# Kernel tuning notes

Hardware: AMD Instinct MI355X
Metric: run time of the kernel (lower is better)

## Reference

```python
import jax, jax.numpy as jnp
import numpy as np

B, S, D, H = 2, 2048, 1024, 16
DK = D // H

def setup_inputs() -> dict:
    key = jax.random.key(0)
    ks = jax.random.split(key, 12)
    def lin(k):
        kw, kb = jax.random.split(k)
        bound = 1.0 / np.sqrt(D)
        W = jax.random.uniform(kw, (D, D), jnp.float32, -bound, bound)
        b = jax.random.uniform(kb, (D,), jnp.float32, -bound, bound)
        return W, b
    Wq, bq = lin(ks[0]); Wk, bk = lin(ks[1]); Wv, bv = lin(ks[2]); Wo, bo = lin(ks[3])
    q = jax.random.normal(ks[4], (B, S, D), jnp.float32)
    k = jax.random.normal(ks[5], (B, S, D), jnp.float32)
    v = jax.random.normal(ks[6], (B, S, D), jnp.float32)
    mask = jnp.ones((1, 1, S, S), jnp.int32)
    return {"q": q, "k": k, "v": v, "mask": mask,
            "Wq": Wq, "bq": bq, "Wk": Wk, "bk": bk,
            "Wv": Wv, "bv": bv, "Wo": Wo, "bo": bo}

def reference(q, k, v, mask, Wq, bq, Wk, bk, Wv, bv, Wo, bo):
    # torch Linear: y = x @ W.T + b
    Q = (q @ Wq.T + bq).reshape(B, S, H, DK).transpose(0, 2, 1, 3)  # [B,H,S,DK]
    K = (k @ Wk.T + bk).reshape(B, S, H, DK).transpose(0, 2, 1, 3)
    V = (v @ Wv.T + bv).reshape(B, S, H, DK).transpose(0, 2, 1, 3)
    scores = jnp.einsum('bhqd,bhkd->bhqk', Q, K) / jnp.sqrt(jnp.float32(DK))
    scores = jnp.where(mask == 0, jnp.float32(-1e9), scores)
    attn = jax.nn.softmax(scores, axis=-1)
    context = jnp.einsum('bhqk,bhkd->bhqd', attn, V)  # [B,H,S,DK]
    concat = context.transpose(0, 2, 1, 3).reshape(B, S, D)
    return concat @ Wo.T + bo
```

## Files before the change

kernel.cpp:

```cpp
#include <hip/hip_runtime.h>
#include <hip/hip_bf16.h>

#define BB 2
#define SS 2048
#define DD 1024
#define HH 16
#define DKK 64

typedef __hip_bfloat16 bf16;
typedef unsigned short u16;
using frag_ab = __attribute__((ext_vector_type(8))) short;
using frag_cd = __attribute__((ext_vector_type(4))) float;

__device__ inline u16 f2bf(float f) {
    bf16 h = __float2bfloat16(f);
    return *reinterpret_cast<u16*>(&h);
}

__device__ inline void gld16(const void* g, void* l) {
    __builtin_amdgcn_global_load_lds((const __attribute__((address_space(1))) void*)g,
                                     (__attribute__((address_space(3))) void*)l,
                                     16, 0, 0);
}

__device__ inline int swz16(int idx) {
    return idx ^ (((idx >> 6) & 7) << 3);
}

__global__ __launch_bounds__(256) void prep(
    const float* __restrict__ q, const float* __restrict__ k, const float* __restrict__ v,
    const float* __restrict__ Wq, const float* __restrict__ Wk,
    const float* __restrict__ Wv, const float* __restrict__ Wo,
    u16* __restrict__ qb, u16* __restrict__ kb, u16* __restrict__ vb,
    u16* __restrict__ Wqb, u16* __restrict__ Wkb, u16* __restrict__ Wvb, u16* __restrict__ Wob,
    const int* __restrict__ mask, int* __restrict__ flags) {
    int bid = blockIdx.x;
    int t = threadIdx.x;
    if (bid < 8192) {
        const float* src;
        u16* dst;
        int local;
        if (bid < 6144) {
            int ts = bid >> 11;
            local = bid & 2047;
            src = ts == 0 ? q : (ts == 1 ? k : v);
            dst = ts == 0 ? qb : (ts == 1 ? kb : vb);
        } else {
            int wsel = (bid - 6144) >> 9;
            local = (bid - 6144) & 511;
            src = wsel == 0 ? Wq : (wsel == 1 ? Wk : (wsel == 2 ? Wv : Wo));
            dst = wsel == 0 ? Wqb : (wsel == 1 ? Wkb : (wsel == 2 ? Wvb : Wob));
        }
        size_t base = (size_t)local * 2048 + t * 8;
        float4 a = *(const float4*)&src[base];
        float4 b = *(const float4*)&src[base + 4];
        ushort4 u0, u1;
        u0.x = f2bf(a.x); u0.y = f2bf(a.y); u0.z = f2bf(a.z); u0.w = f2bf(a.w);
        u1.x = f2bf(b.x); u1.y = f2bf(b.y); u1.z = f2bf(b.z); u1.w = f2bf(b.w);
        *(ushort4*)&dst[base] = u0;
        *(ushort4*)&dst[base + 4] = u1;
    } else {
        int tile = bid - 8192;
        int qt = tile >> 5, kt = tile & 31;
        __shared__ int f;
        if (t == 0) f = 0;
        __syncthreads();
        int qq = qt * 64 + (t >> 2);
        const int4* row = (const int4*)(mask + (size_t)qq * SS + kt * 64 + (t & 3) * 16);
        int anyz = 0;
#pragma unroll
        for (int i = 0; i < 4; ++i) {
            int4 m4 = row[i];
            anyz |= (m4.x == 0) | (m4.y == 0) | (m4.z == 0) | (m4.w == 0);
        }
        if (anyz) f = 1;
        __syncthreads();
        if (t == 0) flags[tile] = f;
    }
}

__global__ __launch_bounds__(256) void qkv_gemm(
    const u16* __restrict__ Aq, const u16* __restrict__ Ak, const u16* __restrict__ Av,
    const u16* __restrict__ Wq, const u16* __restrict__ Wk, const u16* __restrict__ Wv,
    const float* __restrict__ bq, const float* __restrict__ bk, const float* __restrict__ bv,
    u16* __restrict__ Qo, u16* __restrict__ Ko, u16* __restrict__ Vo) {
    __shared__ u16 As[128 * 32];
    __shared__ u16 Bs[128 * 32];

    int z = blockIdx.z;
    const u16* A = z == 0 ? Aq : (z == 1 ? Ak : Av);
    const u16* W = z == 0 ? Wq : (z == 1 ? Wk : Wv);
    const float* bias = z == 0 ? bq : (z == 1 ? bk : bv);
    u16* out = z == 0 ? Qo : (z == 1 ? Ko : Vo);

    int t = threadIdx.x;
    int m0 = blockIdx.y * 128;
    int n0 = blockIdx.x * 128;
    int w = t >> 6, lane = t & 63;
    int quad = lane >> 4, l16 = lane & 15;
    int wm = w >> 1, wn = w & 1;

    const u16* Ab = A + (size_t)m0 * DD;
    const u16* Wb = W + (size_t)n0 * DD;

    frag_cd acc[4][4];
#pragma unroll
    for (int mt = 0; mt < 4; ++mt)
#pragma unroll
        for (int nt = 0; nt < 4; ++nt) acc[mt][nt] = frag_cd{0.f, 0.f, 0.f, 0.f};

    for (int k0 = 0; k0 < DD; k0 += 32) {
        if (k0) __syncthreads();
#pragma unroll
        for (int i = 0; i < 2; ++i) {
            int c = t + i * 256;
            int row = c >> 2, kc = (c & 3) * 8;
            gld16(Ab + (size_t)row * DD + k0 + kc, &As[c * 8]);
            gld16(Wb + (size_t)row * DD + k0 + kc, &Bs[c * 8]);
        }
        __syncthreads();

        frag_ab af[4], bfr[4];
#pragma unroll
        for (int mt = 0; mt < 4; ++mt)
            af[mt] = *(const frag_ab*)&As[(wm * 64 + mt * 16 + l16) * 32 + quad * 8];
#pragma unroll
        for (int nt = 0; nt < 4; ++nt)
            bfr[nt] = *(const frag_ab*)&Bs[(wn * 64 + nt * 16 + l16) * 32 + quad * 8];
#pragma unroll
        for (int mt = 0; mt < 4; ++mt)
#pragma unroll
            for (int nt = 0; nt < 4; ++nt)
                acc[mt][nt] = __builtin_amdgcn_mfma_f32_16x16x32_bf16(
                    af[mt], bfr[nt], acc[mt][nt], 0, 0, 0);
    }

    float scale = z == 0 ? 0.18033688f : 1.0f;
#pragma unroll
    for (int nt = 0; nt < 4; ++nt) {
        int n = n0 + wn * 64 + nt * 16 + l16;
        float bv_ = bias[n];
        int h_ = n >> 6, d_ = n & 63;
#pragma unroll
        for (int mt = 0; mt < 4; ++mt) {
            int mb = m0 + wm * 64 + mt * 16 + quad * 4;
            int b_ = mb >> 11, s_ = mb & 2047;
            if (z == 2) {
                ushort4 u;
                u.x = f2bf(acc[mt][nt][0] + bv_);
                u.y = f2bf(acc[mt][nt][1] + bv_);
                u.z = f2bf(acc[mt][nt][2] + bv_);
                u.w = f2bf(acc[mt][nt][3] + bv_);
                *(ushort4*)&out[((size_t)(b_ * HH + h_) * DKK + d_) * SS + s_] = u;
            } else {
#pragma unroll
                for (int r = 0; r < 4; ++r)
                    out[((size_t)(b_ * HH + h_) * SS + s_ + r) * DKK + d_] =
                        f2bf((acc[mt][nt][r] + bv_) * scale);
            }
        }
    }
}

__global__ __launch_bounds__(256) void out_gemm(const u16* __restrict__ A,
                                                const u16* __restrict__ W,
                                                const float* __restrict__ bias,
                                                float* __restrict__ out) {
    __shared__ u16 As[128 * 32];
    __shared__ u16 Bs[128 * 32];

    int t = threadIdx.x;
    int m0 = blockIdx.y * 128;
    int n0 = blockIdx.x * 128;
    int w = t >> 6, lane = t & 63;
    int quad = lane >> 4, l16 = lane & 15;
    int wm = w >> 1, wn = w & 1;

    const u16* Ab = A + (size_t)m0 * DD;
    const u16* Wb = W + (size_t)n0 * DD;

    frag_cd acc[4][4];
#pragma unroll
    for (int mt = 0; mt < 4; ++mt)
#pragma unroll
        for (int nt = 0; nt < 4; ++nt) acc[mt][nt] = frag_cd{0.f, 0.f, 0.f, 0.f};

    for (int k0 = 0; k0 < DD; k0 += 32) {
        if (k0) __syncthreads();
#pragma unroll
        for (int i = 0; i < 2; ++i) {
            int c = t + i * 256;
            int row = c >> 2, kc = (c & 3) * 8;
            gld16(Ab + (size_t)row * DD + k0 + kc, &As[c * 8]);
            gld16(Wb + (size_t)row * DD + k0 + kc, &Bs[c * 8]);
        }
        __syncthreads();

        frag_ab af[4], bfr[4];
#pragma unroll
        for (int mt = 0; mt < 4; ++mt)
            af[mt] = *(const frag_ab*)&As[(wm * 64 + mt * 16 + l16) * 32 + quad * 8];
#pragma unroll
        for (int nt = 0; nt < 4; ++nt)
            bfr[nt] = *(const frag_ab*)&Bs[(wn * 64 + nt * 16 + l16) * 32 + quad * 8];
#pragma unroll
        for (int mt = 0; mt < 4; ++mt)
#pragma unroll
            for (int nt = 0; nt < 4; ++nt)
                acc[mt][nt] = __builtin_amdgcn_mfma_f32_16x16x32_bf16(
                    af[mt], bfr[nt], acc[mt][nt], 0, 0, 0);
    }

#pragma unroll
    for (int nt = 0; nt < 4; ++nt) {
        int n = n0 + wn * 64 + nt * 16 + l16;
        float bv_ = bias[n];
#pragma unroll
        for (int mt = 0; mt < 4; ++mt) {
            int mb = m0 + wm * 64 + mt * 16 + quad * 4;
#pragma unroll
            for (int r = 0; r < 4; ++r)
                out[(size_t)(mb + r) * DD + n] = acc[mt][nt][r] + bv_;
        }
    }
}

__global__ __launch_bounds__(512) void attn_mfma(const u16* __restrict__ Qb,
                                                 const u16* __restrict__ Kb,
                                                 const u16* __restrict__ Vb,
                                                 const int* __restrict__ mask,
                                                 const int* __restrict__ flags,
                                                 u16* __restrict__ C) {
    __shared__ u16 Ks[64 * 64];
    __shared__ u16 Vt[64 * 64];
    __shared__ u16 Pw[8][16 * 72];

    int blk = blockIdx.x;
    int Qt = blk & 15;
    int bh = blk >> 4;
    int h = bh & 15;
    int b = bh >> 4;
    int q0 = Qt * 128;

    const u16* Kg = Kb + (size_t)bh * SS * DKK;
    const u16* Vg = Vb + (size_t)bh * DKK * SS;

    int t = threadIdx.x;
    int w = t >> 6;
    int lane = t & 63;
    int quad = lane >> 4;
    int l16 = lane & 15;

    frag_ab bq0, bq1;
    {
        const u16* Qr = Qb + ((size_t)bh * SS + q0 + w * 16 + l16) * DKK;
        bq0 = *(const frag_ab*)&Qr[quad * 8];
        bq1 = *(const frag_ab*)&Qr[32 + quad * 8];
    }

    frag_ab ones;
#pragma unroll
    for (int j = 0; j < 8; ++j) ones[j] = (short)0x3F80;

    frag_cd o[4];
#pragma unroll
    for (int dt = 0; dt < 4; ++dt) o[dt] = frag_cd{0.f, 0.f, 0.f, 0.f};
    frag_cd lacc = frag_cd{0.f, 0.f, 0.f, 0.f};
    float m_prev = -1e30f;

    int vd = t >> 3;
    int vc = (t & 7) * 8;
    int fbase = (Qt * 2 + (w >> 2)) * 32;

    unsigned azmask = 0;
#pragma unroll
    for (int i = 0; i < 32; ++i) azmask |= (flags[fbase + i] != 0 ? 1u : 0u) << i;

    int4 kr0, vr0;
    {
        kr0 = ((const int4*)Kg)[t];
        vr0 = *(const int4*)(Vg + (size_t)vd * SS + vc);
    }

    for (int kt = 0; kt < 32; ++kt) {
        if (kt) __syncthreads();
        *(int4*)&Ks[swz16(8 * t)] = kr0;
        *(int4*)&Vt[swz16(vd * 64 + vc)] = vr0;
        if (kt < 31) {
            kr0 = ((const int4*)(Kg + (size_t)(kt + 1) * 4096))[t];
            vr0 = *(const int4*)(Vg + (size_t)vd * SS + (kt + 1) * 64 + vc);
        }
        __syncthreads();

        float s[4][4];
        __builtin_amdgcn_s_setprio(1);
#pragma unroll
        for (int nt = 0; nt < 4; ++nt) {
            int kr = nt * 16 + l16;
            frag_ab ak0 = *(const frag_ab*)&Ks[swz16(kr * 64 + quad * 8)];
            frag_ab ak1 = *(const frag_ab*)&Ks[swz16(kr * 64 + 32 + quad * 8)];
            frag_cd sf = frag_cd{0.f, 0.f, 0.f, 0.f};
            sf = __builtin_amdgcn_mfma_f32_16x16x32_bf16(ak0, bq0, sf, 0, 0, 0);
            sf = __builtin_amdgcn_mfma_f32_16x16x32_bf16(ak1, bq1, sf, 0, 0, 0);
#pragma unroll
            for (int r = 0; r < 4; ++r) s[nt][r] = sf[r];
        }
        __builtin_amdgcn_s_setprio(0);

        if ((azmask >> kt) & 1) {
            int qg = q0 + w * 16 + l16;
#pragma unroll
            for (int nt = 0; nt < 4; ++nt)
#pragma unroll
                for (int r = 0; r < 4; ++r) {
                    int kg = kt * 64 + nt * 16 + quad * 4 + r;
                    if (mask[(size_t)qg * SS + kg] == 0) s[nt][r] = -1e9f;
                }
        }

        float m0_ = fmaxf(fmaxf(s[0][0], s[0][1]), fmaxf(s[0][2], s[0][3]));
        float m1_ = fmaxf(fmaxf(s[1][0], s[1][1]), fmaxf(s[1][2], s[1][3]));
        float m2_ = fmaxf(fmaxf(s[2][0], s[2][1]), fmaxf(s[2][2], s[2][3]));
        float m3_ = fmaxf(fmaxf(s[3][0], s[3][1]), fmaxf(s[3][2], s[3][3]));
        float mc = fmaxf(fmaxf(m0_, m1_), fmaxf(m2_, m3_));
        mc = fmaxf(mc, __shfl_xor(mc, 16));
        mc = fmaxf(mc, __shfl_xor(mc, 32));
        if (!__all(mc <= m_prev + 11.f)) {
            float mnew = fmaxf(m_prev, mc);
            float alpha = exp2f(m_prev - mnew);
#pragma unroll
            for (int r = 0; r < 4; ++r) lacc[r] *= alpha;
#pragma unroll
            for (int dt = 0; dt < 4; ++dt)
#pragma unroll
                for (int r = 0; r < 4; ++r) o[dt][r] *= alpha;
            m_prev = mnew;
        }

        float p[4][4];
#pragma unroll
        for (int nt = 0; nt < 4; ++nt)
#pragma unroll
            for (int r = 0; r < 4; ++r)
                p[nt][r] = exp2f(s[nt][r] - m_prev);

#pragma unroll
        for (int nt = 0; nt < 4; ++nt) {
            ushort4 up;
            up.x = f2bf(p[nt][0]); up.y = f2bf(p[nt][1]);
            up.z = f2bf(p[nt][2]); up.w = f2bf(p[nt][3]);
            *(ushort4*)&Pw[w][l16 * 72 + nt * 16 + quad * 4] = up;
        }
        frag_ab bp0 = *(const frag_ab*)&Pw[w][l16 * 72 + quad * 8];
        frag_ab bp1 = *(const frag_ab*)&Pw[w][l16 * 72 + 32 + quad * 8];

        __builtin_amdgcn_s_setprio(1);
        lacc = __builtin_amdgcn_mfma_f32_16x16x32_bf16(ones, bp0, lacc, 0, 0, 0);
        lacc = __builtin_amdgcn_mfma_f32_16x16x32_bf16(ones, bp1, lacc, 0, 0, 0);
#pragma unroll
        for (int dt = 0; dt < 4; ++dt) {
            int dr = dt * 16 + l16;
            frag_ab av0 = *(const frag_ab*)&Vt[swz16(dr * 64 + quad * 8)];
            frag_ab av1 = *(const frag_ab*)&Vt[swz16(dr * 64 + 32 + quad * 8)];
            o[dt] = __builtin_amdgcn_mfma_f32_16x16x32_bf16(av0, bp0, o[dt], 0, 0, 0);
            o[dt] = __builtin_amdgcn_mfma_f32_16x16x32_bf16(av1, bp1, o[dt], 0, 0, 0);
        }
        __builtin_amdgcn_s_setprio(0);
    }

    {
        float inv = 1.f / lacc[0];
        int qg = q0 + w * 16 + l16;
        u16* Crow = C + ((size_t)b * SS + qg) * DD + h * 64;
#pragma unroll
        for (int dt = 0; dt < 4; ++dt) {
            ushort4 u;
            u.x = f2bf(o[dt][0] * inv);
            u.y = f2bf(o[dt][1] * inv);
            u.z = f2bf(o[dt][2] * inv);
            u.w = f2bf(o[dt][3] * inv);
            *(ushort4*)&Crow[dt * 16 + quad * 4] = u;
        }
    }
}

extern "C" void kernel_launch(void* const* d_in, const int* in_sizes, int n_in,
                              void* d_out, int out_size, void* d_ws, size_t ws_size,
                              hipStream_t stream) {
    const float* q = (const float*)d_in[0];
    const float* k = (const float*)d_in[1];
    const float* v = (const float*)d_in[2];
    const int* mask = (const int*)d_in[3];
    const float* Wq = (const float*)d_in[4];
    const float* bq = (const float*)d_in[5];
    const float* Wk = (const float*)d_in[6];
    const float* bk = (const float*)d_in[7];
    const float* Wv = (const float*)d_in[8];
    const float* bv = (const float*)d_in[9];
    const float* Wo = (const float*)d_in[10];
    const float* bo = (const float*)d_in[11];
    float* out = (float*)d_out;

    const size_t MB = 1024u * 1024u;
    char* ws = (char*)d_ws;
    u16* qb = (u16*)(ws + 0 * MB);
    u16* kb = (u16*)(ws + 8 * MB);
    u16* vb = (u16*)(ws + 16 * MB);
    u16* Wqb = (u16*)(ws + 24 * MB);
    u16* Wkb = (u16*)(ws + 26 * MB);
    u16* Wvb = (u16*)(ws + 28 * MB);
    u16* Wob = (u16*)(ws + 30 * MB);
    u16* Qb = (u16*)(ws + 32 * MB);
    u16* Kb = (u16*)(ws + 40 * MB);
    u16* Vb = (u16*)(ws + 48 * MB);
    int* flags = (int*)(ws + 56 * MB);
    u16* Cw = qb;

    prep<<<9216, 256, 0, stream>>>(q, k, v, Wq, Wk, Wv, Wo,
                                   qb, kb, vb, Wqb, Wkb, Wvb, Wob, mask, flags);

    dim3 grid(DD / 128, (BB * SS) / 128, 3);
    qkv_gemm<<<grid, 256, 0, stream>>>(qb, kb, vb, Wqb, Wkb, Wvb,
                                       bq, bk, bv, Qb, Kb, Vb);

    attn_mfma<<<BB * HH * (SS / 128), 512, 0, stream>>>(Qb, Kb, Vb, mask, flags, Cw);

    out_gemm<<<dim3(DD / 128, (BB * SS) / 128), 256, 0, stream>>>(Cw, Wob, bo, out);
}
```

Measured before the change: 258.5 us.

## Switch attention kernel to 32x32x16 MFMA with 4 waves per block

Rewrites the attention kernel so each wave handles 32 query rows using 32x32x16 bf16 MFMA instead of 16 rows with 16x16x32, halving the block size to 256 threads. Each thread now loads two K/V chunks per tile. The larger MFMA shape gives more reuse per LDS fragment load and fewer instructions per FLOP, but it raises register pressure with three 16-wide accumulators and halves the number of waves per block, which may reduce latency hiding.

```diff
diff --git a/kernel.cpp b/kernel.cpp
--- a/kernel.cpp
+++ b/kernel.cpp
@@ -11,6 +11,7 @@
 typedef unsigned short u16;
 using frag_ab = __attribute__((ext_vector_type(8))) short;
 using frag_cd = __attribute__((ext_vector_type(4))) float;
+using f32x16  = __attribute__((ext_vector_type(16))) float;
 
 __device__ inline u16 f2bf(float f) {
     bf16 h = __float2bfloat16(f);
@@ -225,7 +226,7 @@
     }
 }
 
-__global__ __launch_bounds__(512) void attn_mfma(const u16* __restrict__ Qb,
+__global__ __launch_bounds__(256) void attn_mfma(const u16* __restrict__ Qb,
                                                  const u16* __restrict__ Kb,
                                                  const u16* __restrict__ Vb,
                                                  const int* __restrict__ mask,
@@ -233,7 +234,7 @@
                                                  u16* __restrict__ C) {
     __shared__ u16 Ks[64 * 64];
     __shared__ u16 Vt[64 * 64];
-    __shared__ u16 Pw[8][16 * 72];
+    __shared__ u16 Pw[4][32 * 72];
 
     int blk = blockIdx.x;
     int Qt = blk & 15;
@@ -248,138 +249,154 @@
     int t = threadIdx.x;
     int w = t >> 6;
     int lane = t & 63;
-    int quad = lane >> 4;
-    int l16 = lane & 15;
-
-    frag_ab bq0, bq1;
+    int l32 = lane & 31;
+    int hi = lane >> 5;
+
+    frag_ab bq[4];
     {
-        const u16* Qr = Qb + ((size_t)bh * SS + q0 + w * 16 + l16) * DKK;
-        bq0 = *(const frag_ab*)&Qr[quad * 8];
-        bq1 = *(const frag_ab*)&Qr[32 + quad * 8];
+        const u16* Qr = Qb + ((size_t)bh * SS + q0 + w * 32 + l32) * DKK;
+#pragma unroll
+        for (int ks = 0; ks < 4; ++ks)
+            bq[ks] = *(const frag_ab*)&Qr[ks * 16 + hi * 8];
     }
 
     frag_ab ones;
 #pragma unroll
     for (int j = 0; j < 8; ++j) ones[j] = (short)0x3F80;
 
-    frag_cd o[4];
-#pragma unroll
-    for (int dt = 0; dt < 4; ++dt) o[dt] = frag_cd{0.f, 0.f, 0.f, 0.f};
-    frag_cd lacc = frag_cd{0.f, 0.f, 0.f, 0.f};
+    f32x16 o0, o1, lacc;
+#pragma unroll
+    for (int j = 0; j < 16; ++j) { o0[j] = 0.f; o1[j] = 0.f; lacc[j] = 0.f; }
     float m_prev = -1e30f;
 
-    int vd = t >> 3;
-    int vc = (t & 7) * 8;
-    int fbase = (Qt * 2 + (w >> 2)) * 32;
+    int vd0 = t >> 3;
+    int vc0 = (t & 7) * 8;
+    int fbase = (Qt * 2 + (w >> 1)) * 32;
 
     unsigned azmask = 0;
 #pragma unroll
     for (int i = 0; i < 32; ++i) azmask |= (flags[fbase + i] != 0 ? 1u : 0u) << i;
 
-    int4 kr0, vr0;
+    int4 kr0, kr1, vr0, vr1;
     {
         kr0 = ((const int4*)Kg)[t];
-        vr0 = *(const int4*)(Vg + (size_t)vd * SS + vc);
+        kr1 = ((const int4*)Kg)[t + 256];
+        vr0 = *(const int4*)(Vg + (size_t)vd0 * SS + vc0);
+        vr1 = *(const int4*)(Vg + (size_t)(vd0 + 32) * SS + vc0);
     }
 
     for (int kt = 0; kt < 32; ++kt) {
         if (kt) __syncthreads();
         *(int4*)&Ks[swz16(8 * t)] = kr0;
-        *(int4*)&Vt[swz16(vd * 64 + vc)] = vr0;
+        *(int4*)&Ks[swz16(8 * (t + 256))] = kr1;
+        *(int4*)&Vt[swz16(vd0 * 64 + vc0)] = vr0;
+        *(int4*)&Vt[swz16((vd0 + 32) * 64 + vc0)] = vr1;
         if (kt < 31) {
-            kr0 = ((const int4*)(Kg + (size_t)(kt + 1) * 4096))[t];
-            vr0 = *(const int4*)(Vg + (size_t)vd * SS + (kt + 1) * 64 + vc);
+            const int4* Kt = (const int4*)(Kg + (size_t)(kt + 1) * 4096);
+            kr0 = Kt[t];
+            kr1 = Kt[t + 256];
+            vr0 = *(const int4*)(Vg + (size_t)vd0 * SS + (kt + 1) * 64 + vc0);
+            vr1 = *(const int4*)(Vg + (size_t)(vd0 + 32) * SS + (kt + 1) * 64 + vc0);
         }
         __syncthreads();
 
-        float s[4][4];
+        float s[2][16];
         __builtin_amdgcn_s_setprio(1);
 #pragma unroll
-        for (int nt = 0; nt < 4; ++nt) {
-            int kr = nt * 16 + l16;
-            frag_ab ak0 = *(const frag_ab*)&Ks[swz16(kr * 64 + quad * 8)];
-            frag_ab ak1 = *(const frag_ab*)&Ks[swz16(kr * 64 + 32 + quad * 8)];
-            frag_cd sf = frag_cd{0.f, 0.f, 0.f, 0.f};
-            sf = __builtin_amdgcn_mfma_f32_16x16x32_bf16(ak0, bq0, sf, 0, 0, 0);
-            sf = __builtin_amdgcn_mfma_f32_16x16x32_bf16(ak1, bq1, sf, 0, 0, 0);
-#pragma unroll
-            for (int r = 0; r < 4; ++r) s[nt][r] = sf[r];
+        for (int kb = 0; kb < 2; ++kb) {
+            f32x16 sf;
+#pragma unroll
+            for (int j = 0; j < 16; ++j) sf[j] = 0.f;
+            int kr = kb * 32 + l32;
+#pragma unroll
+            for (int ks = 0; ks < 4; ++ks) {
+                frag_ab ak = *(const frag_ab*)&Ks[swz16(kr * 64 + ks * 16 + hi * 8)];
+                sf = __builtin_amdgcn_mfma_f32_32x32x16_bf16(ak, bq[ks], sf, 0, 0, 0);
+            }
+#pragma unroll
+            for (int r = 0; r < 16; ++r) s[kb][r] = sf[r];
         }
         __builtin_amdgcn_s_setprio(0);
 
         if ((azmask >> kt) & 1) {
-            int qg = q0 + w * 16 + l16;
-#pragma unroll
-            for (int nt = 0; nt < 4; ++nt)
-#pragma unroll
-                for (int r = 0; r < 4; ++r) {
-                    int kg = kt * 64 + nt * 16 + quad * 4 + r;
-                    if (mask[(size_t)qg * SS + kg] == 0) s[nt][r] = -1e9f;
+            int qg = q0 + w * 32 + l32;
+#pragma unroll
+            for (int kb = 0; kb < 2; ++kb)
+#pragma unroll
+                for (int r = 0; r < 16; ++r) {
+                    int kg = kt * 64 + kb * 32 + (r & 3) + 8 * (r >> 2) + 4 * hi;
+                    if (mask[(size_t)qg * SS + kg] == 0) s[kb][r] = -1e9f;
                 }
         }
 
-        float m0_ = fmaxf(fmaxf(s[0][0], s[0][1]), fmaxf(s[0][2], s[0][3]));
-        float m1_ = fmaxf(fmaxf(s[1][0], s[1][1]), fmaxf(s[1][2], s[1][3]));
-        float m2_ = fmaxf(fmaxf(s[2][0], s[2][1]), fmaxf(s[2][2], s[2][3]));
-        float m3_ = fmaxf(fmaxf(s[3][0], s[3][1]), fmaxf(s[3][2], s[3][3]));
-        float mc = fmaxf(fmaxf(m0_, m1_), fmaxf(m2_, m3_));
-        mc = fmaxf(mc, __shfl_xor(mc, 16));
+        float mc = s[0][0];
+#pragma unroll
+        for (int r = 1; r < 16; ++r) mc = fmaxf(mc, s[0][r]);
+#pragma unroll
+        for (int r = 0; r < 16; ++r) mc = fmaxf(mc, s[1][r]);
         mc = fmaxf(mc, __shfl_xor(mc, 32));
         if (!__all(mc <= m_prev + 11.f)) {
             float mnew = fmaxf(m_prev, mc);
             float alpha = exp2f(m_prev - mnew);
 #pragma unroll
-            for (int r = 0; r < 4; ++r) lacc[r] *= alpha;
-#pragma unroll
-            for (int dt = 0; dt < 4; ++dt)
-#pragma unroll
-                for (int r = 0; r < 4; ++r) o[dt][r] *= alpha;
+            for (int j = 0; j < 16; ++j) {
+                lacc[j] *= alpha; o0[j] *= alpha; o1[j] *= alpha;
+            }
             m_prev = mnew;
         }
 
-        float p[4][4];
-#pragma unroll
-        for (int nt = 0; nt < 4; ++nt)
-#pragma unroll
-            for (int r = 0; r < 4; ++r)
-                p[nt][r] = exp2f(s[nt][r] - m_prev);
-
-#pragma unroll
-        for (int nt = 0; nt < 4; ++nt) {
-            ushort4 up;
-            up.x = f2bf(p[nt][0]); up.y = f2bf(p[nt][1]);
-            up.z = f2bf(p[nt][2]); up.w = f2bf(p[nt][3]);
-            *(ushort4*)&Pw[w][l16 * 72 + nt * 16 + quad * 4] = up;
-        }
-        frag_ab bp0 = *(const frag_ab*)&Pw[w][l16 * 72 + quad * 8];
-        frag_ab bp1 = *(const frag_ab*)&Pw[w][l16 * 72 + 32 + quad * 8];
+#pragma unroll
+        for (int kb = 0; kb < 2; ++kb)
+#pragma unroll
+            for (int r = 0; r < 16; ++r)
+                s[kb][r] = exp2f(s[kb][r] - m_prev);
+
+#pragma unroll
+        for (int kb = 0; kb < 2; ++kb)
+#pragma unroll
+            for (int g = 0; g < 4; ++g) {
+                ushort4 up;
+                up.x = f2bf(s[kb][g * 4 + 0]);
+                up.y = f2bf(s[kb][g * 4 + 1]);
+                up.z = f2bf(s[kb][g * 4 + 2]);
+                up.w = f2bf(s[kb][g * 4 + 3]);
+                *(ushort4*)&Pw[w][l32 * 72 + kb * 32 + g * 8 + hi * 4] = up;
+            }
+        frag_ab bp[4];
+#pragma unroll
+        for (int ks2 = 0; ks2 < 4; ++ks2)
+            bp[ks2] = *(const frag_ab*)&Pw[w][l32 * 72 + ks2 * 16 + hi * 8];
 
         __builtin_amdgcn_s_setprio(1);
-        lacc = __builtin_amdgcn_mfma_f32_16x16x32_bf16(ones, bp0, lacc, 0, 0, 0);
-        lacc = __builtin_amdgcn_mfma_f32_16x16x32_bf16(ones, bp1, lacc, 0, 0, 0);
-#pragma unroll
-        for (int dt = 0; dt < 4; ++dt) {
-            int dr = dt * 16 + l16;
-            frag_ab av0 = *(const frag_ab*)&Vt[swz16(dr * 64 + quad * 8)];
-            frag_ab av1 = *(const frag_ab*)&Vt[swz16(dr * 64 + 32 + quad * 8)];
-            o[dt] = __builtin_amdgcn_mfma_f32_16x16x32_bf16(av0, bp0, o[dt], 0, 0, 0);
-            o[dt] = __builtin_amdgcn_mfma_f32_16x16x32_bf16(av1, bp1, o[dt], 0, 0, 0);
+#pragma unroll
+        for (int ks2 = 0; ks2 < 4; ++ks2) {
+            frag_ab av0 = *(const frag_ab*)&Vt[swz16(l32 * 64 + ks2 * 16 + hi * 8)];
+            frag_ab av1 = *(const frag_ab*)&Vt[swz16((32 + l32) * 64 + ks2 * 16 + hi * 8)];
+            o0 = __builtin_amdgcn_mfma_f32_32x32x16_bf16(av0, bp[ks2], o0, 0, 0, 0);
+            o1 = __builtin_amdgcn_mfma_f32_32x32x16_bf16(av1, bp[ks2], o1, 0, 0, 0);
+            lacc = __builtin_amdgcn_mfma_f32_32x32x16_bf16(ones, bp[ks2], lacc, 0, 0, 0);
         }
         __builtin_amdgcn_s_setprio(0);
     }
 
     {
         float inv = 1.f / lacc[0];
-        int qg = q0 + w * 16 + l16;
+        int qg = q0 + w * 32 + l32;
         u16* Crow = C + ((size_t)b * SS + qg) * DD + h * 64;
 #pragma unroll
-        for (int dt = 0; dt < 4; ++dt) {
+        for (int g = 0; g < 4; ++g) {
             ushort4 u;
-            u.x = f2bf(o[dt][0] * inv);
-            u.y = f2bf(o[dt][1] * inv);
-            u.z = f2bf(o[dt][2] * inv);
-            u.w = f2bf(o[dt][3] * inv);
-            *(ushort4*)&Crow[dt * 16 + quad * 4] = u;
+            u.x = f2bf(o0[g * 4 + 0] * inv);
+            u.y = f2bf(o0[g * 4 + 1] * inv);
+            u.z = f2bf(o0[g * 4 + 2] * inv);
+            u.w = f2bf(o0[g * 4 + 3] * inv);
+            *(ushort4*)&Crow[g * 8 + hi * 4] = u;
+            ushort4 u2;
+            u2.x = f2bf(o1[g * 4 + 0] * inv);
+            u2.y = f2bf(o1[g * 4 + 1] * inv);
+            u2.z = f2bf(o1[g * 4 + 2] * inv);
+            u2.w = f2bf(o1[g * 4 + 3] * inv);
+            *(ushort4*)&Crow[32 + g * 8 + hi * 4] = u2;
         }
     }
 }
@@ -423,7 +440,7 @@
     qkv_gemm<<<grid, 256, 0, stream>>>(qb, kb, vb, Wqb, Wkb, Wvb,
                                        bq, bk, bv, Qb, Kb, Vb);
 
-    attn_mfma<<<BB * HH * (SS / 128), 512, 0, stream>>>(Qb, Kb, Vb, mask, flags, Cw);
+    attn_mfma<<<BB * HH * (SS / 128), 256, 0, stream>>>(Qb, Kb, Vb, mask, flags, Cw);
 
     out_gemm<<<dim3(DD / 128, (BB * SS) / 128), 256, 0, stream>>>(Cw, Wob, bo, out);
 }
```

After: 266.5 us. +3.1%, slower.
